# Kernel optimization log

Measured on AMD Instinct MI355X. Metric: run time of the kernel, lower is better.

## Reference

```python
import jax, jax.numpy as jnp
import numpy as np


def setup_inputs() -> dict:
    key = jax.random.key(0)
    k1, k2 = jax.random.split(key)
    N, resolution = 32, 512
    cam2world_matrix = jax.random.normal(k1, (N, 4, 4), dtype=jnp.float32)
    # keep fx, fy (divisors) away from zero
    intrinsics = jax.random.uniform(k2, (N, 3, 3), dtype=jnp.float32, minval=0.5, maxval=1.5)
    return {"cam2world_matrix": cam2world_matrix, "intrinsics": intrinsics, "resolution": resolution}


def reference(cam2world_matrix, intrinsics, resolution):
    # patch_scale=1, masked_sampling=0 default path: full_resolution == resolution
    N = cam2world_matrix.shape[0]
    M = resolution * resolution
    cam_locs_world = cam2world_matrix[:, :3, 3]              # (N, 3)
    fx = intrinsics[:, 0, 0][:, None]
    fy = intrinsics[:, 1, 1][:, None]
    cx = intrinsics[:, 0, 2][:, None]
    cy = intrinsics[:, 1, 2][:, None]
    sk = intrinsics[:, 0, 1][:, None]

    # pixel-center uv grid in [0,1); torch builds (i,j) then flips channels,
    # so x_cam is the flattened column (j) grid, y_cam the row (i) grid.
    coords = (jnp.arange(resolution, dtype=jnp.float32) + 0.5) / resolution
    ii, jj = jnp.meshgrid(coords, coords, indexing='ij')      # (R, R) each
    x_cam = jj.reshape(1, M)                                  # broadcast over N
    y_cam = ii.reshape(1, M)
    z_cam = -1.0                                              # z_cam = -ones

    x_lift = -(x_cam - cx + cy * sk / fy - sk * y_cam / fy) / fx * z_cam  # (N, M)
    y_lift = (y_cam - cy) / fy * z_cam                                    # (N, M)

    ones = jnp.ones((N, M), dtype=cam2world_matrix.dtype)
    cam_rel_points = jnp.stack(
        (jnp.broadcast_to(x_lift, (N, M)),
         jnp.broadcast_to(y_lift, (N, M)),
         -ones, ones), axis=-1)                               # (N, M, 4)

    world_rel_points = jnp.einsum('nij,nmj->nmi', cam2world_matrix, cam_rel_points)[:, :, :3]
    ray_dirs = world_rel_points - cam_locs_world[:, None, :]
    norm = jnp.maximum(jnp.linalg.norm(ray_dirs, axis=2, keepdims=True), 1e-12)
    ray_dirs = ray_dirs / norm
    ray_origins = jnp.broadcast_to(cam_locs_world[:, None, :], ray_dirs.shape)
    return ray_origins, ray_dirs
```

## Files before the change

kernel.cpp:

```cpp
#include <hip/hip_runtime.h>
#include <math.h>

__global__ __launch_bounds__(256) void ray_sampler_kernel(
    const float* __restrict__ c2w,
    const float* __restrict__ intr,
    float* __restrict__ out,
    int M, int res, int blocks_per_n, size_t dir_off)
{
    const int n = blockIdx.x / blocks_per_n;
    const int g = (blockIdx.x % blocks_per_n) * blockDim.x + threadIdx.x;
    const int m0 = g * 8;
    if (m0 >= M) return;

    const float* C = c2w + n * 16;
    const float* K = intr + n * 9;

    const float r00 = C[0], r01 = C[1], r02 = C[2];
    const float ox  = C[3];
    const float r10 = C[4], r11 = C[5], r12 = C[6];
    const float oy  = C[7];
    const float r20 = C[8], r21 = C[9], r22 = C[10];
    const float oz  = C[11];

    const float fx = K[0], sk = K[1], cx = K[2];
    const float fy = K[4], cy = K[5];

    const float inv_fx  = 1.0f / fx;
    const float inv_fy  = 1.0f / fy;
    const float inv_res = 1.0f / (float)res;

    const int i  = m0 / res;
    const int j0 = m0 - i * res;

    const float y_cam  = ((float)i + 0.5f) * inv_res;
    const float ycc    = (y_cam - cy) * inv_fy;
    const float y_lift = -ycc;
    const float xc_off = -cx - sk * ycc;

    const float base0 = r01 * y_lift - r02;
    const float base1 = r11 * y_lift - r12;
    const float base2 = r21 * y_lift - r22;

    float dbuf[24];
    #pragma unroll
    for (int k = 0; k < 8; ++k) {
        const float x_cam  = ((float)(j0 + k) + 0.5f) * inv_res;
        const float x_lift = (x_cam + xc_off) * inv_fx;
        const float dx = fmaf(r00, x_lift, base0);
        const float dy = fmaf(r10, x_lift, base1);
        const float dz = fmaf(r20, x_lift, base2);
        const float s   = fmaf(dx, dx, fmaf(dy, dy, dz * dz));
        const float inv = rsqrtf(fmaxf(s, 1e-24f));
        dbuf[3 * k + 0] = dx * inv;
        dbuf[3 * k + 1] = dy * inv;
        dbuf[3 * k + 2] = dz * inv;
    }

    const size_t base = ((size_t)n * (size_t)M + (size_t)m0) * 3;

    float4* pd = reinterpret_cast<float4*>(out + dir_off + base);
    #pragma unroll
    for (int q = 0; q < 6; ++q)
        pd[q] = make_float4(dbuf[4 * q], dbuf[4 * q + 1], dbuf[4 * q + 2], dbuf[4 * q + 3]);

    const float4 p0 = make_float4(ox, oy, oz, ox);
    const float4 p1 = make_float4(oy, oz, ox, oy);
    const float4 p2 = make_float4(oz, ox, oy, oz);
    float4* po = reinterpret_cast<float4*>(out + base);
    po[0] = p0; po[1] = p1; po[2] = p2;
    po[3] = p0; po[4] = p1; po[5] = p2;
}

extern "C" void kernel_launch(void* const* d_in, const int* in_sizes, int n_in,
                              void* d_out, int out_size, void* d_ws, size_t ws_size,
                              hipStream_t stream) {
    const float* c2w  = (const float*)d_in[0];
    const float* intr = (const float*)d_in[1];
    float* out = (float*)d_out;

    const int N = in_sizes[0] / 16;
    const long long M = (long long)out_size / (6LL * (long long)N);
    const int res = (int)(sqrt((double)M) + 0.5);

    const int groups_per_n = (int)(M / 8);
    const int blocks_per_n = (groups_per_n + 255) / 256;
    const int grid = N * blocks_per_n;
    const size_t dir_off = (size_t)N * (size_t)M * 3;

    ray_sampler_kernel<<<grid, 256, 0, stream>>>(c2w, intr, out,
                                                 (int)M, res, blocks_per_n, dir_off);
}
```

Before: 220.8 us.

## Remap threads so each writes one contiguous float4 of origins and directions

Replaces the per-thread 8-pixel chunk (six strided float4 stores per output) with a mapping where consecutive threads write consecutive float4s. Each thread computes the two pixels its float4 straddles and selects components by phase. This gives fully coalesced stores. It adds redundant per-pixel parameter loads, true divisions and phase-select logic. It also assumes M and res are powers of two, which holds for res=512.

```diff
diff --git a/kernel.cpp b/kernel.cpp
--- a/kernel.cpp
+++ b/kernel.cpp
@@ -1,74 +1,77 @@
 #include <hip/hip_runtime.h>
 #include <math.h>
 
-__global__ __launch_bounds__(256) void ray_sampler_kernel(
+__global__ __launch_bounds__(256) void ray_sampler_contig(
     const float* __restrict__ c2w,
     const float* __restrict__ intr,
     float* __restrict__ out,
-    int M, int res, int blocks_per_n, size_t dir_off)
+    int F4,
+    int mShift,
+    int resShift,
+    float inv_res,
+    size_t dir_off)
 {
-    const int n = blockIdx.x / blocks_per_n;
-    const int g = (blockIdx.x % blocks_per_n) * blockDim.x + threadIdx.x;
-    const int m0 = g * 8;
-    if (m0 >= M) return;
+    const unsigned t = blockIdx.x * 256u + threadIdx.x;
+    if (t >= (unsigned)F4) return;
 
-    const float* C = c2w + n * 16;
-    const float* K = intr + n * 9;
+    const unsigned f0    = t * 4u;
+    const unsigned p0    = f0 / 3u;
+    const unsigned phase = f0 - p0 * 3u;
+    const unsigned Mmask = (1u << mShift) - 1u;
+    const unsigned rmask = (1u << resShift) - 1u;
 
-    const float r00 = C[0], r01 = C[1], r02 = C[2];
-    const float ox  = C[3];
-    const float r10 = C[4], r11 = C[5], r12 = C[6];
-    const float oy  = C[7];
-    const float r20 = C[8], r21 = C[9], r22 = C[10];
-    const float oz  = C[11];
+    float d[6], o[6];
+    #pragma unroll
+    for (int s = 0; s < 2; ++s) {
+        const unsigned p = p0 + (unsigned)s;
+        const unsigned n = p >> mShift;
+        const unsigned m = p & Mmask;
+        const unsigned i = m >> resShift;
+        const unsigned j = m & rmask;
 
-    const float fx = K[0], sk = K[1], cx = K[2];
-    const float fy = K[4], cy = K[5];
+        const float* C = c2w + n * 16;
+        const float* K = intr + n * 9;
 
-    const float inv_fx  = 1.0f / fx;
-    const float inv_fy  = 1.0f / fy;
-    const float inv_res = 1.0f / (float)res;
+        const float r00 = C[0], r01 = C[1], r02 = C[2];
+        const float r10 = C[4], r11 = C[5], r12 = C[6];
+        const float r20 = C[8], r21 = C[9], r22 = C[10];
+        o[3 * s + 0] = C[3];
+        o[3 * s + 1] = C[7];
+        o[3 * s + 2] = C[11];
 
-    const int i  = m0 / res;
-    const int j0 = m0 - i * res;
+        const float fx = K[0], sk = K[1], cx = K[2];
+        const float fy = K[4], cy = K[5];
 
-    const float y_cam  = ((float)i + 0.5f) * inv_res;
-    const float ycc    = (y_cam - cy) * inv_fy;
-    const float y_lift = -ycc;
-    const float xc_off = -cx - sk * ycc;
+        const float y_cam  = ((float)i + 0.5f) * inv_res;
+        const float ycc    = (y_cam - cy) / fy;
+        const float y_lift = -ycc;
+        const float xc_off = -cx - sk * ycc;
+        const float x_cam  = ((float)j + 0.5f) * inv_res;
+        const float x_lift = (x_cam + xc_off) / fx;
 
-    const float base0 = r01 * y_lift - r02;
-    const float base1 = r11 * y_lift - r12;
-    const float base2 = r21 * y_lift - r22;
+        const float dx = fmaf(r00, x_lift, fmaf(r01, y_lift, -r02));
+        const float dy = fmaf(r10, x_lift, fmaf(r11, y_lift, -r12));
+        const float dz = fmaf(r20, x_lift, fmaf(r21, y_lift, -r22));
+        const float ss  = fmaf(dx, dx, fmaf(dy, dy, dz * dz));
+        const float inv = rsqrtf(fmaxf(ss, 1e-24f));
 
-    float dbuf[24];
-    #pragma unroll
-    for (int k = 0; k < 8; ++k) {
-        const float x_cam  = ((float)(j0 + k) + 0.5f) * inv_res;
-        const float x_lift = (x_cam + xc_off) * inv_fx;
-        const float dx = fmaf(r00, x_lift, base0);
-        const float dy = fmaf(r10, x_lift, base1);
-        const float dz = fmaf(r20, x_lift, base2);
-        const float s   = fmaf(dx, dx, fmaf(dy, dy, dz * dz));
-        const float inv = rsqrtf(fmaxf(s, 1e-24f));
-        dbuf[3 * k + 0] = dx * inv;
-        dbuf[3 * k + 1] = dy * inv;
-        dbuf[3 * k + 2] = dz * inv;
+        d[3 * s + 0] = dx * inv;
+        d[3 * s + 1] = dy * inv;
+        d[3 * s + 2] = dz * inv;
     }
 
-    const size_t base = ((size_t)n * (size_t)M + (size_t)m0) * 3;
+    float4 vo, vd;
+    vo.x = (phase == 0) ? o[0] : ((phase == 1) ? o[1] : o[2]);
+    vo.y = (phase == 0) ? o[1] : ((phase == 1) ? o[2] : o[3]);
+    vo.z = (phase == 0) ? o[2] : ((phase == 1) ? o[3] : o[4]);
+    vo.w = (phase == 0) ? o[3] : ((phase == 1) ? o[4] : o[5]);
+    vd.x = (phase == 0) ? d[0] : ((phase == 1) ? d[1] : d[2]);
+    vd.y = (phase == 0) ? d[1] : ((phase == 1) ? d[2] : d[3]);
+    vd.z = (phase == 0) ? d[2] : ((phase == 1) ? d[3] : d[4]);
+    vd.w = (phase == 0) ? d[3] : ((phase == 1) ? d[4] : d[5]);
 
-    float4* pd = reinterpret_cast<float4*>(out + dir_off + base);
-    #pragma unroll
-    for (int q = 0; q < 6; ++q)
-        pd[q] = make_float4(dbuf[4 * q], dbuf[4 * q + 1], dbuf[4 * q + 2], dbuf[4 * q + 3]);
-
-    const float4 p0 = make_float4(ox, oy, oz, ox);
-    const float4 p1 = make_float4(oy, oz, ox, oy);
-    const float4 p2 = make_float4(oz, ox, oy, oz);
-    float4* po = reinterpret_cast<float4*>(out + base);
-    po[0] = p0; po[1] = p1; po[2] = p2;
-    po[3] = p0; po[4] = p1; po[5] = p2;
+    reinterpret_cast<float4*>(out)[t]           = vo;
+    reinterpret_cast<float4*>(out + dir_off)[t] = vd;
 }
 
 extern "C" void kernel_launch(void* const* d_in, const int* in_sizes, int n_in,
@@ -82,11 +85,15 @@
     const long long M = (long long)out_size / (6LL * (long long)N);
     const int res = (int)(sqrt((double)M) + 0.5);
 
-    const int groups_per_n = (int)(M / 8);
-    const int blocks_per_n = (groups_per_n + 255) / 256;
-    const int grid = N * blocks_per_n;
-    const size_t dir_off = (size_t)N * (size_t)M * 3;
+    int mShift = 0;   while ((1LL << mShift) < M)  ++mShift;
+    int resShift = 0; while ((1 << resShift) < res) ++resShift;
 
-    ray_sampler_kernel<<<grid, 256, 0, stream>>>(c2w, intr, out,
-                                                 (int)M, res, blocks_per_n, dir_off);
+    const long long F  = (long long)N * M * 3LL;
+    const int F4       = (int)(F / 4);
+    const int grid     = (F4 + 255) / 256;
+    const size_t dir_off = (size_t)F;
+
+    ray_sampler_contig<<<grid, 256, 0, stream>>>(c2w, intr, out,
+                                                 F4, mShift, resShift,
+                                                 1.0f / (float)res, dir_off);
 }
```

New measurement: 206.9 us. 1.07x faster.
